# Performance work log

Hardware: AMD Instinct MI355X
Metric: run time of the kernel (lower is better)

Reference implementation:

```python
import jax, jax.numpy as jnp
import numpy as np

B, N, C, H, M = 32, 256, 1024, 16, 77
DH = C // H
W = int(N ** 0.5)
MLP_H = 4 * C

def _rel_index(w):
    ch = np.arange(w)
    coords = np.stack(np.meshgrid(ch, ch, indexing='ij'))  # [2, w, w]
    cf = coords.reshape(2, -1)
    rc = (cf[:, :, None] - cf[:, None, :]).transpose(1, 2, 0).astype(np.int64)
    rc[..., 0] += w - 1
    rc[..., 1] += w - 1
    rc[..., 0] *= 2 * w - 1
    return jnp.asarray(rc.sum(-1))  # [N, N]

REL_IDX = _rel_index(W)

def setup_inputs():
    key = jax.random.key(0)
    ks = jax.random.split(key, 12)
    p = lambda k, sh: jax.random.normal(k, sh, jnp.float32) * 0.02
    return dict(
        x=jax.random.normal(ks[0], (B, N, C), jnp.float32),
        noise_level=jax.random.normal(ks[1], (B, C), jnp.float32),
        y=jax.random.normal(ks[2], (B, M, C), jnp.float32),
        W_qkv=p(ks[3], (C, 3 * C)), b_qkv=jnp.zeros((3 * C,), jnp.float32),
        W_proj=p(ks[4], (C, C)), b_proj=jnp.zeros((C,), jnp.float32),
        rel_table=p(ks[5], ((2 * W - 1) ** 2 + 3, H)),
        W_ada=p(ks[6], (C, 6 * C)), b_ada=jnp.zeros((6 * C,), jnp.float32),
        W_fc1=p(ks[7], (C, MLP_H)), b_fc1=jnp.zeros((MLP_H,), jnp.float32),
        W_fc2=p(ks[8], (MLP_H, C)), b_fc2=jnp.zeros((C,), jnp.float32),
        W_q=p(ks[9], (C, C)), W_kv=p(ks[10], (C, 2 * C)),
    )

def _ln(x):
    # LayerNorm without affine, eps=1e-6, biased variance (matches torch)
    mu = x.mean(-1, keepdims=True)
    var = x.var(-1, keepdims=True)
    return (x - mu) * jax.lax.rsqrt(var + 1e-6)

def _modulate(x, shift, scale):
    return x * (1 + scale[:, None, :]) + shift[:, None, :]

def reference(x, noise_level, y, W_qkv, b_qkv, W_proj, b_proj, rel_table,
              W_ada, b_ada, W_fc1, b_fc1, W_fc2, b_fc2, W_q, W_kv):
    ada = jax.nn.silu(noise_level) @ W_ada + b_ada  # [B, 6C]
    sh_msa, sc_msa, g_msa, sh_mlp, sc_mlp, g_mlp = jnp.split(ada, 6, axis=1)

    # --- self-attention with relative position bias (heads split as (h d)) ---
    h = _modulate(_ln(x), sh_msa, sc_msa)
    qkv = (h @ W_qkv + b_qkv).reshape(B, N, 3, H, DH)
    q, k, v = qkv[:, :, 0], qkv[:, :, 1], qkv[:, :, 2]  # [B, N, H, DH]
    bias = rel_table[REL_IDX].transpose(2, 0, 1)  # [H, N, N]
    scores = jnp.einsum('bnhd,bmhd->bhnm', q, k) * (DH ** -0.5) + bias[None]
    attn = jax.nn.softmax(scores, axis=-1)
    o = jnp.einsum('bhnm,bmhd->bnhd', attn, v).reshape(B, N, C)
    x = x + g_msa[:, None, :] * (o @ W_proj + b_proj)

    # --- cross attention; einops '(d h)' split: head index is the FAST axis ---
    q2 = (x @ W_q).reshape(B, N, DH, H)
    kv = y @ W_kv
    k2 = kv[..., :C].reshape(B, M, DH, H)
    v2 = kv[..., C:].reshape(B, M, DH, H)
    s2 = jnp.einsum('bndh,bmdh->bhnm', q2, k2) * (DH ** -0.5)
    a2 = jax.nn.softmax(s2, axis=-1)
    o2 = jnp.einsum('bhnm,bmdh->bndh', a2, v2).reshape(B, N, C)
    x = x + o2

    # --- adaLN-modulated MLP with tanh-approx GELU ---
    h = _modulate(_ln(x), sh_mlp, sc_mlp)
    h = jax.nn.gelu(h @ W_fc1 + b_fc1, approximate=True) @ W_fc2 + b_fc2
    return x + g_mlp[:, None, :] * h
```

## Files before the change

kernel.cpp:

```cpp
#include <hip/hip_runtime.h>
#include <hip/hip_bf16.h>
#include <stdint.h>

typedef __hip_bfloat16 bf16;
using bf16x8 = __attribute__((ext_vector_type(8))) short;
using f32x4  = __attribute__((ext_vector_type(4))) float;


__device__ __forceinline__ void gload_lds16(const void* g, void* l) {
  using gchar = __attribute__((address_space(1))) char;
  using lchar = __attribute__((address_space(3))) char;
  gchar* gp = reinterpret_cast<gchar*>(reinterpret_cast<uintptr_t>(g));
  lchar* lp = reinterpret_cast<lchar*>(static_cast<uint32_t>(reinterpret_cast<uintptr_t>(l)));
  __builtin_amdgcn_global_load_lds(gp, lp, 16, 0, 0);
}

__device__ __forceinline__ unsigned short f2bf_bits(float x) {
  uint32_t u = __float_as_uint(x);
  uint32_t r = (u + 0x7fffu + ((u >> 16) & 1u)) >> 16;
  return (unsigned short)r;
}

template <int PERM>
__global__ __launch_bounds__(256) void transpose_bf16(
    const float* __restrict__ W, bf16* __restrict__ Wt, int K, int N) {
  __shared__ float t[32][33];
  const int n0 = blockIdx.x * 32, k0 = blockIdx.y * 32;
  const int tx = threadIdx.x & 31, ty = threadIdx.x >> 5;
  #pragma unroll
  for (int i = ty; i < 32; i += 8) t[i][tx] = W[(size_t)(k0 + i) * N + n0 + tx];
  __syncthreads();
  #pragma unroll
  for (int i = ty; i < 32; i += 8) {
    int n = n0 + i;
    int np;
    if constexpr (PERM == 0) np = n;
    else if constexpr (PERM == 1) np = (n & 15) * 64 + (n >> 4);
    else { int base = n & 1024, m = n & 1023; np = base + (m & 15) * 64 + (m >> 4); }
    Wt[(size_t)np * K + k0 + tx] = __float2bfloat16(t[tx][i]);
  }
}

__global__ __launch_bounds__(256) void conv_y(
    const float* __restrict__ y, bf16* __restrict__ yb) {
  int i = blockIdx.x * 256 + threadIdx.x;
  float v = (i < 2464 * 1024) ? y[i] : 0.f;
  yb[i] = __float2bfloat16(v);
}

__global__ __launch_bounds__(256) void silu_pad(
    const float* __restrict__ noise, bf16* __restrict__ Apad) {
  int i = blockIdx.x * 256 + threadIdx.x;
  float v = 0.f;
  if (i < 32 * 1024) {
    float x = noise[i];
    v = x / (1.f + __expf(-x));
  }
  Apad[i] = __float2bfloat16(v);
}

__global__ __launch_bounds__(256) void ln_mod(
    const float* __restrict__ x, const float* __restrict__ ada,
    int shOff, int scOff, bf16* __restrict__ out) {
  const int row = blockIdx.x, b = row >> 8, tid = threadIdx.x;
  const float* xr = x + (size_t)row * 1024;
  float v[4], s = 0.f, ss = 0.f;
  #pragma unroll
  for (int i = 0; i < 4; ++i) {
    v[i] = xr[tid + i * 256];
    s += v[i]; ss += v[i] * v[i];
  }
  #pragma unroll
  for (int o = 32; o; o >>= 1) { s += __shfl_xor(s, o); ss += __shfl_xor(ss, o); }
  __shared__ float red[8];
  const int w = tid >> 6;
  if ((tid & 63) == 0) { red[w] = s; red[w + 4] = ss; }
  __syncthreads();
  s = red[0] + red[1] + red[2] + red[3];
  ss = red[4] + red[5] + red[6] + red[7];
  float mu = s * (1.f / 1024.f);
  float var = ss * (1.f / 1024.f) - mu * mu;
  float rstd = rsqrtf(var + 1e-6f);
  const float* adab = ada + (size_t)b * 6144;
  #pragma unroll
  for (int i = 0; i < 4; ++i) {
    int c = tid + i * 256;
    float o = (v[i] - mu) * rstd * (1.f + adab[scOff + c]) + adab[shOff + c];
    out[(size_t)row * 1024 + c] = __float2bfloat16(o);
  }
}

enum { EPI_STORE = 0, EPI_GELU = 1, EPI_PROJ = 2, EPI_OUT = 3, EPI_ADAF = 4 };

template <int EPI>
__global__ __launch_bounds__(256, 2) void gemm_bf16(
    const bf16* __restrict__ A, const bf16* __restrict__ Bt,
    int N, int K, int gx, int grpG, int xcdP,
    const float* __restrict__ bias, const float* __restrict__ ada, int adaOff,
    const float* __restrict__ resid, float* __restrict__ outF,
    bf16* __restrict__ outB) {
  __shared__ bf16 As[128 * 64];
  __shared__ bf16 Bs[128 * 64];
  const int tid = threadIdx.x;
  const int w = tid >> 6, lane = tid & 63;
  const int wr = w >> 1, wc = w & 1;
  const int lr = lane >> 4, lc = lane & 15;

  const int flat = blockIdx.x;
  const int xcd = flat & 7, j = flat >> 3;
  const int cpg = gx / grpG;
  const int grp = xcd / xcdP, par = xcd % xcdP;
  const int bx = grp * cpg + j % cpg;
  const int by = (j / cpg) * xcdP + par;
  const int mBase = by * 128, nBase = bx * 128;

  f32x4 acc[4][4];
  #pragma unroll
  for (int mi = 0; mi < 4; ++mi)
    #pragma unroll
    for (int ni = 0; ni < 4; ++ni)
      #pragma unroll
      for (int j2 = 0; j2 < 4; ++j2) acc[mi][ni][j2] = 0.f;

  const int nK = K >> 6;
  for (int ks = 0; ks < nK; ++ks) {
    const int k0 = ks << 6;
    #pragma unroll
    for (int i = 0; i < 4; ++i) {
      int t16 = w * 256 + i * 64 + lane;
      int row = t16 >> 3;
      int cL = ((t16 & 7) ^ (row & 7)) << 3;
      gload_lds16(A + (size_t)(mBase + row) * K + k0 + cL, (char*)As + t16 * 16);
      gload_lds16(Bt + (size_t)(nBase + row) * K + k0 + cL, (char*)Bs + t16 * 16);
    }
    __syncthreads();
    #pragma unroll
    for (int kk = 0; kk < 2; ++kk) {
      bf16x8 af[4], bfr[4];
      #pragma unroll
      for (int mi = 0; mi < 4; ++mi) {
        int row = wr * 64 + mi * 16 + lc;
        int byte = row * 128 + ((kk * 64 + lr * 16) ^ ((row & 7) << 4));
        af[mi] = *reinterpret_cast<const bf16x8*>((const char*)As + byte);
      }
      #pragma unroll
      for (int ni = 0; ni < 4; ++ni) {
        int row = wc * 64 + ni * 16 + lc;
        int byte = row * 128 + ((kk * 64 + lr * 16) ^ ((row & 7) << 4));
        bfr[ni] = *reinterpret_cast<const bf16x8*>((const char*)Bs + byte);
      }
      #pragma unroll
      for (int mi = 0; mi < 4; ++mi)
        #pragma unroll
        for (int ni = 0; ni < 4; ++ni)
          acc[mi][ni] = __builtin_amdgcn_mfma_f32_16x16x32_bf16(
              af[mi], bfr[ni], acc[mi][ni], 0, 0, 0);
    }
    __syncthreads();
  }

  const int rB = mBase + wr * 64, cB = nBase + wc * 64;
  #pragma unroll
  for (int mi = 0; mi < 4; ++mi) {
    #pragma unroll
    for (int ni = 0; ni < 4; ++ni) {
      #pragma unroll
      for (int j2 = 0; j2 < 4; ++j2) {
        int r = rB + mi * 16 + lr * 4 + j2;
        int c = cB + ni * 16 + lc;
        float v = acc[mi][ni][j2];
        if (bias) v += bias[c];
        if constexpr (EPI == EPI_STORE) {
          outB[(size_t)r * N + c] = __float2bfloat16(v);
        } else if constexpr (EPI == EPI_GELU) {
          float e = __expf(1.5957691216057308f * v + 0.07135481627260086f * v * v * v);
          float t = 1.f - 2.f / (e + 1.f);
          outB[(size_t)r * N + c] = __float2bfloat16(0.5f * v * (1.f + t));
        } else if constexpr (EPI == EPI_PROJ) {
          int b = r >> 8;
          float g = ada[(size_t)b * 6144 + adaOff + c];
          float o = resid[(size_t)r * 1024 + c] + g * v;
          outF[(size_t)r * 1024 + c] = o;
          outB[(size_t)r * 1024 + c] = __float2bfloat16(o);
        } else if constexpr (EPI == EPI_OUT) {
          int b = r >> 8;
          float g = ada[(size_t)b * 6144 + adaOff + c];
          outF[(size_t)r * 1024 + c] = resid[(size_t)r * 1024 + c] + g * v;
        } else {
          if (r < 32) outF[(size_t)r * N + c] = v;
        }
      }
    }
  }
}

template <int EPI>
__global__ __launch_bounds__(512, 1) void gemm256_bf16(
    const bf16* __restrict__ A, const bf16* __restrict__ Bt,
    int N, int K, int gx, int grpG, int xcdP,
    const float* __restrict__ bias, bf16* __restrict__ outB) {
  __shared__ bf16 As[2 * 256 * 64];
  __shared__ bf16 Bs[2 * 256 * 64];
  const int tid = threadIdx.x;
  const int w = tid >> 6, lane = tid & 63;
  const int wr = w >> 2, wcn = w & 3;
  const int lr = lane >> 4, lc = lane & 15;

  const int flat = blockIdx.x;
  const int xcd = flat & 7, jj = flat >> 3;
  const int cpg = gx / grpG;
  const int grp = xcd / xcdP, par = xcd % xcdP;
  const int bx = grp * cpg + jj % cpg;
  const int by = (jj / cpg) * xcdP + par;
  const int mBase = by * 256, nBase = bx * 256;

  f32x4 acc[8][4];
  #pragma unroll
  for (int mi = 0; mi < 8; ++mi)
    #pragma unroll
    for (int ni = 0; ni < 4; ++ni)
      acc[mi][ni] = f32x4{0.f, 0.f, 0.f, 0.f};

  const int nT = K >> 6;

  auto STAGE = [&](int t, int bufI) {
    const int k0 = t << 6;
    char* Ad = (char*)As + bufI * 32768;
    char* Bd = (char*)Bs + bufI * 32768;
    #pragma unroll
    for (int i = 0; i < 4; ++i) {
      int ck = i * 512 + tid;
      int row = ck >> 3;
      int sc = ((ck & 7) ^ (row & 7)) << 3;
      gload_lds16(A + (size_t)(mBase + row) * K + k0 + sc, Ad + ck * 16);
      gload_lds16(Bt + (size_t)(nBase + row) * K + k0 + sc, Bd + ck * 16);
    }
  };

  STAGE(0, 0);
  STAGE(1, 1);
  asm volatile("s_waitcnt vmcnt(8)" ::: "memory");
  __builtin_amdgcn_sched_barrier(0);
  __builtin_amdgcn_s_barrier();
  __builtin_amdgcn_sched_barrier(0);

  for (int t = 0; t < nT; ++t) {
    const int cur = t & 1;
    const char* Ab = (const char*)As + cur * 32768;
    const char* Bb = (const char*)Bs + cur * 32768;
    bf16x8 af[2][8], bfr[2][4];
    #pragma unroll
    for (int kk = 0; kk < 2; ++kk) {
      #pragma unroll
      for (int mi = 0; mi < 8; ++mi) {
        int row = wr * 128 + mi * 16 + lc;
        int byte = row * 128 + ((kk * 64 + lr * 16) ^ ((row & 7) << 4));
        af[kk][mi] = *reinterpret_cast<const bf16x8*>(Ab + byte);
      }
      #pragma unroll
      for (int ni = 0; ni < 4; ++ni) {
        int row = wcn * 64 + ni * 16 + lc;
        int byte = row * 128 + ((kk * 64 + lr * 16) ^ ((row & 7) << 4));
        bfr[kk][ni] = *reinterpret_cast<const bf16x8*>(Bb + byte);
      }
    }
    asm volatile("s_waitcnt lgkmcnt(0)" ::: "memory");
    __builtin_amdgcn_sched_barrier(0);
    __builtin_amdgcn_s_barrier();
    __builtin_amdgcn_sched_barrier(0);

    if (t + 2 < nT) STAGE(t + 2, cur);

    __builtin_amdgcn_s_setprio(1);
    #pragma unroll
    for (int kk = 0; kk < 2; ++kk)
      #pragma unroll
      for (int mi = 0; mi < 8; ++mi)
        #pragma unroll
        for (int ni = 0; ni < 4; ++ni)
          acc[mi][ni] = __builtin_amdgcn_mfma_f32_16x16x32_bf16(
              af[kk][mi], bfr[kk][ni], acc[mi][ni], 0, 0, 0);
    __builtin_amdgcn_s_setprio(0);

    if (t < nT - 1) {
      if (t + 2 < nT) {
        asm volatile("s_waitcnt vmcnt(8)" ::: "memory");
      } else {
        asm volatile("s_waitcnt vmcnt(0)" ::: "memory");
      }
      __builtin_amdgcn_sched_barrier(0);
      __builtin_amdgcn_s_barrier();
      __builtin_amdgcn_sched_barrier(0);
    }
  }

  const int rB = mBase + wr * 128, cB = nBase + wcn * 64;
  #pragma unroll
  for (int mi = 0; mi < 8; ++mi) {
    #pragma unroll
    for (int ni = 0; ni < 4; ++ni) {
      #pragma unroll
      for (int j2 = 0; j2 < 4; ++j2) {
        int r = rB + mi * 16 + lr * 4 + j2;
        int c = cB + ni * 16 + lc;
        float v = acc[mi][ni][j2] + bias[c];
        if constexpr (EPI == EPI_STORE) {
          outB[(size_t)r * N + c] = __float2bfloat16(v);
        } else {
          float e = __expf(1.5957691216057308f * v + 0.07135481627260086f * v * v * v);
          float t2 = 1.f - 2.f / (e + 1.f);
          outB[(size_t)r * N + c] = __float2bfloat16(0.5f * v * (1.f + t2));
        }
      }
    }
  }
}

__global__ __launch_bounds__(512, 1) void attn1_mfma(
    const bf16* __restrict__ qkv, const float* __restrict__ rel,
    bf16* __restrict__ o) {
  __shared__ bf16 Ks[256 * 64];
  __shared__ bf16 Vt[64 * 256];
  __shared__ ushort Pl[8][32 * 40];
  __shared__ float bias_s[964];

  const int tid = threadIdx.x;
  const int w = tid >> 6, lane = tid & 63;
  const int p4 = lane >> 4, c = lane & 15;
  const int bh = blockIdx.x, b = bh >> 4, h = bh & 15;
  const bf16* basep = qkv + (size_t)b * 256 * 3072 + h * 64;

  #pragma unroll
  for (int it = 0; it < 4; ++it) {
    int t16 = it * 512 + tid;
    int row = t16 >> 3;
    int sc = ((t16 & 7) ^ (row & 7)) << 3;
    gload_lds16(basep + (size_t)row * 3072 + 1024 + sc, (char*)Ks + t16 * 16);
  }
  #pragma unroll
  for (int it = 0; it < 4; ++it) {
    int i = it * 512 + tid;
    int key = i >> 3, d0 = (i & 7) * 8;
    int4 u = *reinterpret_cast<const int4*>(basep + (size_t)key * 3072 + 2048 + d0);
    const ushort* us = reinterpret_cast<const ushort*>(&u);
    #pragma unroll
    for (int j = 0; j < 8; ++j) {
      int dh = d0 + j;
      int byte = dh * 512 + ((key * 2) ^ ((dh & 7) << 4));
      *reinterpret_cast<ushort*>((char*)Vt + byte) = us[j];
    }
  }
  for (int i = tid; i < 964; i += 512) bias_s[i] = rel[i * 16 + h];

  bf16x8 qf[2][2];
  #pragma unroll
  for (int mi = 0; mi < 2; ++mi)
    #pragma unroll
    for (int s = 0; s < 2; ++s) {
      int q = w * 32 + mi * 16 + c;
      int dh = s * 32 + p4 * 8;
      int4 u = *reinterpret_cast<const int4*>(basep + (size_t)q * 3072 + dh);
      uint32_t a[4] = {(uint32_t)u.x, (uint32_t)u.y, (uint32_t)u.z, (uint32_t)u.w};
      bf16x8 r;
      #pragma unroll
      for (int t = 0; t < 4; ++t) {
        float lo = __uint_as_float(a[t] << 16) * 0.125f;
        float hi = __uint_as_float(a[t] & 0xffff0000u) * 0.125f;
        r[2 * t]     = (short)(__float_as_uint(lo) >> 16);
        r[2 * t + 1] = (short)(__float_as_uint(hi) >> 16);
      }
      qf[mi][s] = r;
    }
  __syncthreads();

  float m_run[2][4], l_run[2][4];
  f32x4 oacc[2][4];
  #pragma unroll
  for (int mi = 0; mi < 2; ++mi)
    #pragma unroll
    for (int j = 0; j < 4; ++j) {
      m_run[mi][j] = -1e30f; l_run[mi][j] = 0.f;
      oacc[mi][j] = f32x4{0.f, 0.f, 0.f, 0.f};
    }

  ushort* Pw = &Pl[w][0];
  const int colterm = p4 * 4 - c + 15;

  for (int kt = 0; kt < 8; ++kt) {
    f32x4 sacc[2][2];
    #pragma unroll
    for (int mi = 0; mi < 2; ++mi)
      #pragma unroll
      for (int nf = 0; nf < 2; ++nf) {
        int bi = ((w * 2 + mi) - (kt * 2 + nf) + 15) * 31 + colterm;
        #pragma unroll
        for (int j = 0; j < 4; ++j) sacc[mi][nf][j] = bias_s[bi + j];
      }
    #pragma unroll
    for (int nf = 0; nf < 2; ++nf) {
      int key = kt * 32 + nf * 16 + c;
      #pragma unroll
      for (int s = 0; s < 2; ++s) {
        int byte = key * 128 + (((s * 4 + p4) ^ (key & 7)) << 4);
        bf16x8 kb = *reinterpret_cast<const bf16x8*>((const char*)Ks + byte);
        #pragma unroll
        for (int mi = 0; mi < 2; ++mi)
          sacc[mi][nf] = __builtin_amdgcn_mfma_f32_16x16x32_bf16(
              qf[mi][s], kb, sacc[mi][nf], 0, 0, 0);
      }
    }
    float sf[2][4];
    #pragma unroll
    for (int mi = 0; mi < 2; ++mi)
      #pragma unroll
      for (int j = 0; j < 4; ++j) {
        float cm = fmaxf(sacc[mi][0][j], sacc[mi][1][j]);
        cm = fmaxf(cm, __shfl_xor(cm, 1));
        cm = fmaxf(cm, __shfl_xor(cm, 2));
        cm = fmaxf(cm, __shfl_xor(cm, 4));
        cm = fmaxf(cm, __shfl_xor(cm, 8));
        float nm = fmaxf(m_run[mi][j], cm);
        sf[mi][j] = __expf(m_run[mi][j] - nm);
        m_run[mi][j] = nm;
        l_run[mi][j] *= sf[mi][j];
      }
    #pragma unroll
    for (int mi = 0; mi < 2; ++mi)
      #pragma unroll
      for (int nf = 0; nf < 4; ++nf)
        #pragma unroll
        for (int j = 0; j < 4; ++j) oacc[mi][nf][j] *= sf[mi][j];
    #pragma unroll
    for (int mi = 0; mi < 2; ++mi) {
      #pragma unroll
      for (int nf = 0; nf < 2; ++nf)
        #pragma unroll
        for (int j = 0; j < 4; ++j)
          sacc[mi][nf][j] = __expf(sacc[mi][nf][j] - m_run[mi][j]);
      #pragma unroll
      for (int j = 0; j < 4; ++j) {
        float lp = sacc[mi][0][j] + sacc[mi][1][j];
        lp += __shfl_xor(lp, 1);
        lp += __shfl_xor(lp, 2);
        lp += __shfl_xor(lp, 4);
        lp += __shfl_xor(lp, 8);
        l_run[mi][j] += lp;
      }
      #pragma unroll
      for (int nf = 0; nf < 2; ++nf)
        #pragma unroll
        for (int j = 0; j < 4; ++j)
          Pw[(mi * 16 + p4 * 4 + j) * 40 + nf * 16 + c] =
              f2bf_bits(sacc[mi][nf][j]);
    }
    bf16x8 pa[2], vb[4];
    #pragma unroll
    for (int mi = 0; mi < 2; ++mi)
      pa[mi] = *reinterpret_cast<const bf16x8*>(
          (const char*)Pw + (mi * 16 + c) * 80 + p4 * 16);
    #pragma unroll
    for (int nf = 0; nf < 4; ++nf) {
      int dh = nf * 16 + c;
      int byte = dh * 512 + (((kt * 4 + p4) ^ (dh & 7)) << 4);
      vb[nf] = *reinterpret_cast<const bf16x8*>((const char*)Vt + byte);
    }
    #pragma unroll
    for (int mi = 0; mi < 2; ++mi)
      #pragma unroll
      for (int nf = 0; nf < 4; ++nf)
        oacc[mi][nf] = __builtin_amdgcn_mfma_f32_16x16x32_bf16(
            pa[mi], vb[nf], oacc[mi][nf], 0, 0, 0);
  }

  #pragma unroll
  for (int mi = 0; mi < 2; ++mi) {
    float inv[4];
    #pragma unroll
    for (int j = 0; j < 4; ++j) inv[j] = 1.f / l_run[mi][j];
    #pragma unroll
    for (int nf = 0; nf < 4; ++nf)
      #pragma unroll
      for (int j = 0; j < 4; ++j) {
        int q = w * 32 + mi * 16 + p4 * 4 + j;
        int dh = nf * 16 + c;
        o[((size_t)b * 256 + q) * 1024 + h * 64 + dh] =
            __float2bfloat16(oacc[mi][nf][j] * inv[j]);
      }
  }
}

__global__ __launch_bounds__(512, 1) void attn2_mfma(
    const bf16* __restrict__ q2, const bf16* __restrict__ kv,
    bf16* __restrict__ o2) {
  __shared__ bf16 Ks[80 * 64];
  __shared__ bf16 Vt[64 * 128];
  __shared__ ushort Pl[8][32 * 104];

  const int tid = threadIdx.x;
  const int w = tid >> 6, lane = tid & 63;
  const int p4 = lane >> 4, c = lane & 15;
  const int bh = blockIdx.x, b = bh >> 4, h = bh & 15;
  const size_t kvrow0 = (size_t)b * 77;

  {
    int t16 = tid;
    int key = t16 >> 3;
    int sc = ((t16 & 7) ^ (key & 7)) << 3;
    gload_lds16(kv + (kvrow0 + key) * 2048 + h * 64 + sc, (char*)Ks + t16 * 16);
    if (tid < 128) {
      int u16 = 512 + tid; key = u16 >> 3;
      sc = ((u16 & 7) ^ (key & 7)) << 3;
      gload_lds16(kv + (kvrow0 + key) * 2048 + h * 64 + sc, (char*)Ks + u16 * 16);
    }
  }
  for (int i = tid; i < 80 * 8; i += 512) {
    int key = i >> 3, d0 = (i & 7) * 8;
    int4 u = *reinterpret_cast<const int4*>(
        kv + (kvrow0 + key) * 2048 + 1024 + h * 64 + d0);
    const ushort* us = reinterpret_cast<const ushort*>(&u);
    #pragma unroll
    for (int j = 0; j < 8; ++j) {
      int dh = d0 + j;
      int byte = dh * 256 + ((key * 2) ^ ((dh & 7) << 4));
      *reinterpret_cast<ushort*>((char*)Vt + byte) = us[j];
    }
  }
  {
    int row = lane >> 1, colb = 160 + (lane & 1) * 16;
    *reinterpret_cast<int4*>((char*)&Pl[w][0] + row * 208 + colb) =
        int4{0, 0, 0, 0};
  }
  bf16x8 qf[2][2];
  #pragma unroll
  for (int mi = 0; mi < 2; ++mi)
    #pragma unroll
    for (int s = 0; s < 2; ++s) {
      int q = w * 32 + mi * 16 + c;
      int dh = s * 32 + p4 * 8;
      int4 u = *reinterpret_cast<const int4*>(
          q2 + ((size_t)b * 256 + q) * 1024 + h * 64 + dh);
      uint32_t a[4] = {(uint32_t)u.x, (uint32_t)u.y, (uint32_t)u.z, (uint32_t)u.w};
      bf16x8 r;
      #pragma unroll
      for (int t = 0; t < 4; ++t) {
        float lo = __uint_as_float(a[t] << 16) * 0.125f;
        float hi = __uint_as_float(a[t] & 0xffff0000u) * 0.125f;
        r[2 * t]     = (short)(__float_as_uint(lo) >> 16);
        r[2 * t + 1] = (short)(__float_as_uint(hi) >> 16);
      }
      qf[mi][s] = r;
    }
  __syncthreads();

  f32x4 sacc[2][5];
  #pragma unroll
  for (int mi = 0; mi < 2; ++mi)
    #pragma unroll
    for (int nf = 0; nf < 5; ++nf)
      sacc[mi][nf] = f32x4{0.f, 0.f, 0.f, 0.f};
  #pragma unroll
  for (int nf = 0; nf < 5; ++nf) {
    int key = nf * 16 + c;
    #pragma unroll
    for (int s = 0; s < 2; ++s) {
      int byte = key * 128 + (((s * 4 + p4) ^ (key & 7)) << 4);
      bf16x8 kb = *reinterpret_cast<const bf16x8*>((const char*)Ks + byte);
      #pragma unroll
      for (int mi = 0; mi < 2; ++mi)
        sacc[mi][nf] = __builtin_amdgcn_mfma_f32_16x16x32_bf16(
            qf[mi][s], kb, sacc[mi][nf], 0, 0, 0);
    }
  }
  if (c >= 13) {
    #pragma unroll
    for (int mi = 0; mi < 2; ++mi)
      #pragma unroll
      for (int j = 0; j < 4; ++j) sacc[mi][4][j] = -1e30f;
  }
  float lrow[2][4];
  #pragma unroll
  for (int mi = 0; mi < 2; ++mi)
    #pragma unroll
    for (int j = 0; j < 4; ++j) {
      float cm = sacc[mi][0][j];
      #pragma unroll
      for (int nf = 1; nf < 5; ++nf) cm = fmaxf(cm, sacc[mi][nf][j]);
      cm = fmaxf(cm, __shfl_xor(cm, 1));
      cm = fmaxf(cm, __shfl_xor(cm, 2));
      cm = fmaxf(cm, __shfl_xor(cm, 4));
      cm = fmaxf(cm, __shfl_xor(cm, 8));
      float lp = 0.f;
      #pragma unroll
      for (int nf = 0; nf < 5; ++nf) {
        sacc[mi][nf][j] = __expf(sacc[mi][nf][j] - cm);
        lp += sacc[mi][nf][j];
      }
      lp += __shfl_xor(lp, 1);
      lp += __shfl_xor(lp, 2);
      lp += __shfl_xor(lp, 4);
      lp += __shfl_xor(lp, 8);
      lrow[mi][j] = lp;
    }
  ushort* Pw = &Pl[w][0];
  #pragma unroll
  for (int mi = 0; mi < 2; ++mi)
    #pragma unroll
    for (int nf = 0; nf < 5; ++nf)
      #pragma unroll
      for (int j = 0; j < 4; ++j)
        Pw[(mi * 16 + p4 * 4 + j) * 104 + nf * 16 + c] =
            f2bf_bits(sacc[mi][nf][j]);
  f32x4 oacc[2][4];
  #pragma unroll
  for (int mi = 0; mi < 2; ++mi)
    #pragma unroll
    for (int nf = 0; nf < 4; ++nf) oacc[mi][nf] = f32x4{0.f, 0.f, 0.f, 0.f};
  #pragma unroll
  for (int kk = 0; kk < 3; ++kk) {
    bf16x8 pa[2], vb[4];
    #pragma unroll
    for (int mi = 0; mi < 2; ++mi)
      pa[mi] = *reinterpret_cast<const bf16x8*>(
          (const char*)Pw + (mi * 16 + c) * 208 + kk * 64 + p4 * 16);
    #pragma unroll
    for (int nf = 0; nf < 4; ++nf) {
      int dh = nf * 16 + c;
      int byte = dh * 256 + (((kk * 4 + p4) ^ (dh & 7)) << 4);
      vb[nf] = *reinterpret_cast<const bf16x8*>((const char*)Vt + byte);
    }
    #pragma unroll
    for (int mi = 0; mi < 2; ++mi)
      #pragma unroll
      for (int nf = 0; nf < 4; ++nf)
        oacc[mi][nf] = __builtin_amdgcn_mfma_f32_16x16x32_bf16(
            pa[mi], vb[nf], oacc[mi][nf], 0, 0, 0);
  }
  #pragma unroll
  for (int mi = 0; mi < 2; ++mi) {
    float inv[4];
    #pragma unroll
    for (int j = 0; j < 4; ++j) inv[j] = 1.f / lrow[mi][j];
    #pragma unroll
    for (int nf = 0; nf < 4; ++nf)
      #pragma unroll
      for (int j = 0; j < 4; ++j) {
        int q = w * 32 + mi * 16 + p4 * 4 + j;
        int dh = nf * 16 + c;
        o2[((size_t)b * 256 + q) * 1024 + h * 64 + dh] =
            __float2bfloat16(oacc[mi][nf][j] * inv[j]);
      }
  }
}

__global__ __launch_bounds__(256) void permute_add(
    const bf16* __restrict__ o2, float* __restrict__ xcur) {
  __shared__ float s_lds[1088];
  const int tid = threadIdx.x;
  const int row0 = blockIdx.x * 4;
  for (int r = 0; r < 4; ++r) {
    const int row = row0 + r;
    #pragma unroll
    for (int i = 0; i < 4; ++i) {
      int cc = i * 256 + tid;
      float v = __bfloat162float(o2[(size_t)row * 1024 + cc]);
      s_lds[cc + (cc >> 4)] = v;
    }
    __syncthreads();
    float4 add;
    #pragma unroll
    for (int t = 0; t < 4; ++t) {
      int ct = tid * 4 + t;
      int src = (ct & 15) * 64 + (ct >> 4);
      (&add.x)[t] = s_lds[src + (src >> 4)];
    }
    float4* xp = reinterpret_cast<float4*>(xcur + (size_t)row * 1024 + tid * 4);
    float4 cur = *xp;
    cur.x += add.x; cur.y += add.y; cur.z += add.z; cur.w += add.w;
    *xp = cur;
    __syncthreads();
  }
}


extern "C" void kernel_launch(void* const* d_in, const int* in_sizes, int n_in,
                              void* d_out, int out_size, void* d_ws, size_t ws_size,
                              hipStream_t stream) {
  (void)in_sizes; (void)n_in; (void)out_size; (void)ws_size;
  const float* x      = (const float*)d_in[0];
  const float* noise  = (const float*)d_in[1];
  const float* y      = (const float*)d_in[2];
  const float* W_qkv  = (const float*)d_in[3];
  const float* b_qkv  = (const float*)d_in[4];
  const float* W_proj = (const float*)d_in[5];
  const float* b_proj = (const float*)d_in[6];
  const float* rel    = (const float*)d_in[7];
  const float* W_ada  = (const float*)d_in[8];
  const float* b_ada  = (const float*)d_in[9];
  const float* W_fc1  = (const float*)d_in[10];
  const float* b_fc1  = (const float*)d_in[11];
  const float* W_fc2  = (const float*)d_in[12];
  const float* b_fc2  = (const float*)d_in[13];
  const float* W_q    = (const float*)d_in[14];
  const float* W_kv   = (const float*)d_in[15];

  char* ws = (char*)d_ws;
  size_t off = 0;
  auto alloc = [&](size_t bytes) {
    char* p = ws + off;
    off = (off + bytes + 255) & ~(size_t)255;
    return p;
  };
  float* ada   = (float*)alloc(32u * 6144 * 4);
  float* xcur  = (float*)alloc(8192u * 1024 * 4);
  bf16* WqkvT  = (bf16*)alloc(3072u * 1024 * 2);
  bf16* WprojT = (bf16*)alloc(1024u * 1024 * 2);
  bf16* WqT    = (bf16*)alloc(1024u * 1024 * 2);
  bf16* WkvT   = (bf16*)alloc(2048u * 1024 * 2);
  bf16* Wfc1T  = (bf16*)alloc(4096u * 1024 * 2);
  bf16* Wfc2T  = (bf16*)alloc(1024u * 4096 * 2);
  bf16* WadaT  = (bf16*)alloc(6144u * 1024 * 2);
  bf16* Apad   = (bf16*)alloc(128u * 1024 * 2);
  bf16* hbuf   = (bf16*)alloc(8192u * 1024 * 2);
  bf16* big    = (bf16*)alloc(8192u * 4096 * 2);
  bf16* obuf   = (bf16*)alloc(8192u * 1024 * 2);
  bf16* kvbuf  = (bf16*)alloc(2560u * 2048 * 2);
  bf16* ybuf   = (bf16*)alloc(2560u * 1024 * 2);
  float* outF  = (float*)d_out;

  transpose_bf16<0><<<dim3(96, 32), 256, 0, stream>>>(W_qkv, WqkvT, 1024, 3072);
  transpose_bf16<0><<<dim3(32, 32), 256, 0, stream>>>(W_proj, WprojT, 1024, 1024);
  transpose_bf16<1><<<dim3(32, 32), 256, 0, stream>>>(W_q, WqT, 1024, 1024);
  transpose_bf16<2><<<dim3(64, 32), 256, 0, stream>>>(W_kv, WkvT, 1024, 2048);
  transpose_bf16<0><<<dim3(128, 32), 256, 0, stream>>>(W_fc1, Wfc1T, 1024, 4096);
  transpose_bf16<0><<<dim3(32, 128), 256, 0, stream>>>(W_fc2, Wfc2T, 4096, 1024);
  transpose_bf16<0><<<dim3(192, 32), 256, 0, stream>>>(W_ada, WadaT, 1024, 6144);
  conv_y<<<2560 * 1024 / 256, 256, 0, stream>>>(y, ybuf);

  silu_pad<<<512, 256, 0, stream>>>(noise, Apad);
  gemm_bf16<EPI_ADAF><<<48, 256, 0, stream>>>(
      Apad, WadaT, 6144, 1024, 48, 8, 1, b_ada, nullptr, 0, nullptr, ada, nullptr);

  ln_mod<<<8192, 256, 0, stream>>>(x, ada, 0, 1024, hbuf);
  gemm256_bf16<EPI_STORE><<<384, 512, 0, stream>>>(
      hbuf, WqkvT, 3072, 1024, 12, 4, 2, b_qkv, big);
  attn1_mfma<<<512, 512, 0, stream>>>(big, rel, obuf);
  gemm_bf16<EPI_PROJ><<<512, 256, 0, stream>>>(
      obuf, WprojT, 1024, 1024, 8, 1, 8, b_proj, ada, 2048, x, xcur, hbuf);

  gemm_bf16<EPI_STORE><<<512, 256, 0, stream>>>(
      hbuf, WqT, 1024, 1024, 8, 1, 8, nullptr, nullptr, 0, nullptr, nullptr, obuf);
  gemm_bf16<EPI_STORE><<<320, 256, 0, stream>>>(
      ybuf, WkvT, 2048, 1024, 16, 8, 1, nullptr, nullptr, 0, nullptr, nullptr, kvbuf);
  attn2_mfma<<<512, 512, 0, stream>>>(obuf, kvbuf, big);
  permute_add<<<2048, 256, 0, stream>>>(big, xcur);

  ln_mod<<<8192, 256, 0, stream>>>(xcur, ada, 3072, 4096, hbuf);
  gemm256_bf16<EPI_GELU><<<512, 512, 0, stream>>>(
      hbuf, Wfc1T, 4096, 1024, 16, 4, 2, b_fc1, big);
  gemm_bf16<EPI_OUT><<<512, 256, 0, stream>>>(
      big, Wfc2T, 1024, 4096, 8, 1, 8, b_fc2, ada, 5120, xcur, outF, nullptr);
}
```

Before: 518.1 us.

## Replace 256-tile GEMM with 8-phase interleaved pipeline and reuse it for proj/fc2

Rewrites the 256x256 bf16 GEMM as a templated kernel that splits each K-tile's A and B loads into four half-tile stages. Those stages are interleaved with four MFMA quarter-phases separated by barriers, so global-to-LDS traffic overlaps compute at finer granularity. The kernel also gets a 256x128 variant (NI=2) with the PROJ/OUT/STORE epilogues, replacing the older 256-thread gemm for the proj, q and fc2 GEMMs. The intent is better latency hiding and larger tiles with more reuse, at the cost of many more barriers and fewer blocks for the N=1024 GEMMs.

```diff
diff --git a/kernel.cpp b/kernel.cpp
--- a/kernel.cpp
+++ b/kernel.cpp
@@ -194,122 +194,193 @@
   }
 }
 
-template <int EPI>
-__global__ __launch_bounds__(512, 1) void gemm256_bf16(
+template <int EPI, int NI>
+__global__ __launch_bounds__(512, 1) void gemm8p(
     const bf16* __restrict__ A, const bf16* __restrict__ Bt,
     int N, int K, int gx, int grpG, int xcdP,
-    const float* __restrict__ bias, bf16* __restrict__ outB) {
-  __shared__ bf16 As[2 * 256 * 64];
-  __shared__ bf16 Bs[2 * 256 * 64];
+    const float* __restrict__ bias, const float* __restrict__ ada, int adaOff,
+    const float* __restrict__ resid, float* __restrict__ outF,
+    bf16* __restrict__ outB) {
+  constexpr int BHALF = NI * 32;
+  constexpr int NB_LOADS = NI / 2;
+  __shared__ bf16 AS[2 * 2 * 128 * 64];
+  __shared__ bf16 BS[2 * 2 * BHALF * 64];
+
   const int tid = threadIdx.x;
   const int w = tid >> 6, lane = tid & 63;
-  const int wr = w >> 2, wcn = w & 3;
+  const int wr = w >> 2, wc = w & 3;
   const int lr = lane >> 4, lc = lane & 15;
 
   const int flat = blockIdx.x;
   const int xcd = flat & 7, jj = flat >> 3;
   const int cpg = gx / grpG;
-  const int grp = xcd / xcdP, par = xcd % xcdP;
+  const int grp = xcd / xcdP, par_ = xcd % xcdP;
   const int bx = grp * cpg + jj % cpg;
-  const int by = (jj / cpg) * xcdP + par;
-  const int mBase = by * 256, nBase = bx * 256;
-
-  f32x4 acc[8][4];
+  const int by = (jj / cpg) * xcdP + par_;
+  const int mBase = by * 256, nBase = bx * (NI * 64);
+
+  const int nT = K >> 6;
+
+  f32x4 acc[8][NI];
   #pragma unroll
   for (int mi = 0; mi < 8; ++mi)
     #pragma unroll
-    for (int ni = 0; ni < 4; ++ni)
-      acc[mi][ni] = f32x4{0.f, 0.f, 0.f, 0.f};
-
-  const int nT = K >> 6;
-
-  auto STAGE = [&](int t, int bufI) {
-    const int k0 = t << 6;
-    char* Ad = (char*)As + bufI * 32768;
-    char* Bd = (char*)Bs + bufI * 32768;
-    #pragma unroll
-    for (int i = 0; i < 4; ++i) {
-      int ck = i * 512 + tid;
-      int row = ck >> 3;
-      int sc = ((ck & 7) ^ (row & 7)) << 3;
-      gload_lds16(A + (size_t)(mBase + row) * K + k0 + sc, Ad + ck * 16);
-      gload_lds16(Bt + (size_t)(nBase + row) * K + k0 + sc, Bd + ck * 16);
+    for (int ni = 0; ni < NI; ++ni) acc[mi][ni] = f32x4{0.f, 0.f, 0.f, 0.f};
+
+  auto STAGE = [&](int h) {
+    if (h >= 4 * nT) return;
+    const int th = h >> 2, j = h & 3, par = th & 1;
+    const int k0 = th << 6;
+    if (j < 2) {
+      char* dst = (char*)AS + par * 32768 + j * 16384;
+      #pragma unroll
+      for (int i = 0; i < 2; ++i) {
+        int ck = i * 512 + tid;
+        int row = ck >> 3, c = ck & 7;
+        int col = k0 + ((c ^ (row & 7)) << 3);
+        gload_lds16(A + (size_t)(mBase + j * 128 + row) * K + col, dst + ck * 16);
+      }
+    } else {
+      const int rh = j - 2;
+      char* dst = (char*)BS + par * (BHALF * 256) + rh * (BHALF * 128);
+      #pragma unroll
+      for (int i = 0; i < NB_LOADS; ++i) {
+        int ck = i * 512 + tid;
+        int row = ck >> 3, c = ck & 7;
+        int col = k0 + ((c ^ (row & 7)) << 3);
+        gload_lds16(Bt + (size_t)(nBase + rh * BHALF + row) * K + col, dst + ck * 16);
+      }
     }
   };
 
-  STAGE(0, 0);
-  STAGE(1, 1);
-  asm volatile("s_waitcnt vmcnt(8)" ::: "memory");
-  __builtin_amdgcn_sched_barrier(0);
-  __builtin_amdgcn_s_barrier();
-  __builtin_amdgcn_sched_barrier(0);
+  STAGE(0); STAGE(1); STAGE(2); STAGE(3); STAGE(4); STAGE(5);
 
   for (int t = 0; t < nT; ++t) {
-    const int cur = t & 1;
-    const char* Ab = (const char*)As + cur * 32768;
-    const char* Bb = (const char*)Bs + cur * 32768;
-    bf16x8 af[2][8], bfr[2][4];
-    #pragma unroll
-    for (int kk = 0; kk < 2; ++kk) {
-      #pragma unroll
-      for (int mi = 0; mi < 8; ++mi) {
-        int row = wr * 128 + mi * 16 + lc;
-        int byte = row * 128 + ((kk * 64 + lr * 16) ^ ((row & 7) << 4));
-        af[kk][mi] = *reinterpret_cast<const bf16x8*>(Ab + byte);
-      }
-      #pragma unroll
-      for (int ni = 0; ni < 4; ++ni) {
-        int row = wcn * 64 + ni * 16 + lc;
-        int byte = row * 128 + ((kk * 64 + lr * 16) ^ ((row & 7) << 4));
-        bfr[kk][ni] = *reinterpret_cast<const bf16x8*>(Bb + byte);
-      }
-    }
+    if (t == nT - 1) { asm volatile("s_waitcnt vmcnt(0)" ::: "memory"); }
+    else            { asm volatile("s_waitcnt vmcnt(4)" ::: "memory"); }
+    __builtin_amdgcn_sched_barrier(0);
+    __builtin_amdgcn_s_barrier();
+    __builtin_amdgcn_sched_barrier(0);
+
+    const char* Ab = (const char*)AS + (t & 1) * 32768 + wr * 16384;
+    const char* Bb = (const char*)BS + (t & 1) * (BHALF * 256) + (wc >> 1) * (BHALF * 128);
+
+    bf16x8 af[2][8], bfr[2][NI];
+
+    #pragma unroll
+    for (int mi = 0; mi < 8; ++mi) {
+      int r = mi * 16 + lc;
+      af[0][mi] = *reinterpret_cast<const bf16x8*>(
+          Ab + r * 128 + ((lr * 16) ^ ((r & 7) << 4)));
+    }
+    #pragma unroll
+    for (int ni = 0; ni < NI; ++ni) {
+      int r = (wc * (NI * 16) + ni * 16 + lc) & (BHALF - 1);
+      bfr[0][ni] = *reinterpret_cast<const bf16x8*>(
+          Bb + r * 128 + ((lr * 16) ^ ((r & 7) << 4)));
+    }
+    STAGE(4 * t + 6);
+    __builtin_amdgcn_sched_barrier(0);
+    __builtin_amdgcn_s_barrier();
     asm volatile("s_waitcnt lgkmcnt(0)" ::: "memory");
     __builtin_amdgcn_sched_barrier(0);
+    __builtin_amdgcn_s_setprio(1);
+    #pragma unroll
+    for (int mi = 0; mi < 8; ++mi)
+      #pragma unroll
+      for (int ni = 0; ni < NI / 2; ++ni)
+        acc[mi][ni] = __builtin_amdgcn_mfma_f32_16x16x32_bf16(
+            af[0][mi], bfr[0][ni], acc[mi][ni], 0, 0, 0);
+    __builtin_amdgcn_s_setprio(0);
+    __builtin_amdgcn_sched_barrier(0);
     __builtin_amdgcn_s_barrier();
-    __builtin_amdgcn_sched_barrier(0);
-
-    if (t + 2 < nT) STAGE(t + 2, cur);
-
+
+    #pragma unroll
+    for (int mi = 0; mi < 8; ++mi) {
+      int r = mi * 16 + lc;
+      af[1][mi] = *reinterpret_cast<const bf16x8*>(
+          Ab + r * 128 + ((64 + lr * 16) ^ ((r & 7) << 4)));
+    }
+    #pragma unroll
+    for (int ni = 0; ni < NI; ++ni) {
+      int r = (wc * (NI * 16) + ni * 16 + lc) & (BHALF - 1);
+      bfr[1][ni] = *reinterpret_cast<const bf16x8*>(
+          Bb + r * 128 + ((64 + lr * 16) ^ ((r & 7) << 4)));
+    }
+    STAGE(4 * t + 7);
+    __builtin_amdgcn_sched_barrier(0);
+    __builtin_amdgcn_s_barrier();
+    asm volatile("s_waitcnt lgkmcnt(0)" ::: "memory");
+    __builtin_amdgcn_sched_barrier(0);
     __builtin_amdgcn_s_setprio(1);
     #pragma unroll
-    for (int kk = 0; kk < 2; ++kk)
-      #pragma unroll
-      for (int mi = 0; mi < 8; ++mi)
-        #pragma unroll
-        for (int ni = 0; ni < 4; ++ni)
-          acc[mi][ni] = __builtin_amdgcn_mfma_f32_16x16x32_bf16(
-              af[kk][mi], bfr[kk][ni], acc[mi][ni], 0, 0, 0);
+    for (int mi = 0; mi < 8; ++mi)
+      #pragma unroll
+      for (int ni = NI / 2; ni < NI; ++ni)
+        acc[mi][ni] = __builtin_amdgcn_mfma_f32_16x16x32_bf16(
+            af[0][mi], bfr[0][ni], acc[mi][ni], 0, 0, 0);
     __builtin_amdgcn_s_setprio(0);
-
-    if (t < nT - 1) {
-      if (t + 2 < nT) {
-        asm volatile("s_waitcnt vmcnt(8)" ::: "memory");
-      } else {
-        asm volatile("s_waitcnt vmcnt(0)" ::: "memory");
-      }
-      __builtin_amdgcn_sched_barrier(0);
-      __builtin_amdgcn_s_barrier();
-      __builtin_amdgcn_sched_barrier(0);
-    }
-  }
-
-  const int rB = mBase + wr * 128, cB = nBase + wcn * 64;
+    __builtin_amdgcn_sched_barrier(0);
+    __builtin_amdgcn_s_barrier();
+
+    STAGE(4 * t + 8);
+    __builtin_amdgcn_sched_barrier(0);
+    __builtin_amdgcn_s_barrier();
+    __builtin_amdgcn_sched_barrier(0);
+    __builtin_amdgcn_s_setprio(1);
+    #pragma unroll
+    for (int mi = 0; mi < 8; ++mi)
+      #pragma unroll
+      for (int ni = 0; ni < NI / 2; ++ni)
+        acc[mi][ni] = __builtin_amdgcn_mfma_f32_16x16x32_bf16(
+            af[1][mi], bfr[1][ni], acc[mi][ni], 0, 0, 0);
+    __builtin_amdgcn_s_setprio(0);
+    __builtin_amdgcn_sched_barrier(0);
+    __builtin_amdgcn_s_barrier();
+
+    STAGE(4 * t + 9);
+    __builtin_amdgcn_sched_barrier(0);
+    __builtin_amdgcn_s_barrier();
+    __builtin_amdgcn_sched_barrier(0);
+    __builtin_amdgcn_s_setprio(1);
+    #pragma unroll
+    for (int mi = 0; mi < 8; ++mi)
+      #pragma unroll
+      for (int ni = NI / 2; ni < NI; ++ni)
+        acc[mi][ni] = __builtin_amdgcn_mfma_f32_16x16x32_bf16(
+            af[1][mi], bfr[1][ni], acc[mi][ni], 0, 0, 0);
+    __builtin_amdgcn_s_setprio(0);
+    __builtin_amdgcn_sched_barrier(0);
+    __builtin_amdgcn_s_barrier();
+  }
+
+  const int rB = mBase + wr * 128, cB = nBase + wc * (NI * 16);
   #pragma unroll
   for (int mi = 0; mi < 8; ++mi) {
     #pragma unroll
-    for (int ni = 0; ni < 4; ++ni) {
+    for (int ni = 0; ni < NI; ++ni) {
       #pragma unroll
       for (int j2 = 0; j2 < 4; ++j2) {
         int r = rB + mi * 16 + lr * 4 + j2;
         int c = cB + ni * 16 + lc;
-        float v = acc[mi][ni][j2] + bias[c];
+        float v = acc[mi][ni][j2];
+        if (bias) v += bias[c];
         if constexpr (EPI == EPI_STORE) {
           outB[(size_t)r * N + c] = __float2bfloat16(v);
-        } else {
+        } else if constexpr (EPI == EPI_GELU) {
           float e = __expf(1.5957691216057308f * v + 0.07135481627260086f * v * v * v);
           float t2 = 1.f - 2.f / (e + 1.f);
           outB[(size_t)r * N + c] = __float2bfloat16(0.5f * v * (1.f + t2));
+        } else if constexpr (EPI == EPI_PROJ) {
+          int b = r >> 8;
+          float g = ada[(size_t)b * 6144 + adaOff + c];
+          float o = resid[(size_t)r * 1024 + c] + g * v;
+          outF[(size_t)r * 1024 + c] = o;
+          outB[(size_t)r * 1024 + c] = __float2bfloat16(o);
+        } else if constexpr (EPI == EPI_OUT) {
+          int b = r >> 8;
+          float g = ada[(size_t)b * 6144 + adaOff + c];
+          outF[(size_t)r * 1024 + c] = resid[(size_t)r * 1024 + c] + g * v;
         }
       }
     }
@@ -741,13 +812,13 @@
       Apad, WadaT, 6144, 1024, 48, 8, 1, b_ada, nullptr, 0, nullptr, ada, nullptr);
 
   ln_mod<<<8192, 256, 0, stream>>>(x, ada, 0, 1024, hbuf);
-  gemm256_bf16<EPI_STORE><<<384, 512, 0, stream>>>(
-      hbuf, WqkvT, 3072, 1024, 12, 4, 2, b_qkv, big);
+  gemm8p<EPI_STORE, 4><<<384, 512, 0, stream>>>(
+      hbuf, WqkvT, 3072, 1024, 12, 4, 2, b_qkv, nullptr, 0, nullptr, nullptr, big);
   attn1_mfma<<<512, 512, 0, stream>>>(big, rel, obuf);
-  gemm_bf16<EPI_PROJ><<<512, 256, 0, stream>>>(
+  gemm8p<EPI_PROJ, 2><<<256, 512, 0, stream>>>(
       obuf, WprojT, 1024, 1024, 8, 1, 8, b_proj, ada, 2048, x, xcur, hbuf);
 
-  gemm_bf16<EPI_STORE><<<512, 256, 0, stream>>>(
+  gemm8p<EPI_STORE, 2><<<256, 512, 0, stream>>>(
       hbuf, WqT, 1024, 1024, 8, 1, 8, nullptr, nullptr, 0, nullptr, nullptr, obuf);
   gemm_bf16<EPI_STORE><<<320, 256, 0, stream>>>(
       ybuf, WkvT, 2048, 1024, 16, 8, 1, nullptr, nullptr, 0, nullptr, nullptr, kvbuf);
@@ -755,8 +826,8 @@
   permute_add<<<2048, 256, 0, stream>>>(big, xcur);
 
   ln_mod<<<8192, 256, 0, stream>>>(xcur, ada, 3072, 4096, hbuf);
-  gemm256_bf16<EPI_GELU><<<512, 512, 0, stream>>>(
-      hbuf, Wfc1T, 4096, 1024, 16, 4, 2, b_fc1, big);
-  gemm_bf16<EPI_OUT><<<512, 256, 0, stream>>>(
+  gemm8p<EPI_GELU, 4><<<512, 512, 0, stream>>>(
+      hbuf, Wfc1T, 4096, 1024, 16, 4, 2, b_fc1, nullptr, 0, nullptr, nullptr, big);
+  gemm8p<EPI_OUT, 2><<<256, 512, 0, stream>>>(
       big, Wfc2T, 1024, 4096, 8, 1, 8, b_fc2, ada, 5120, xcur, outF, nullptr);
 }
```

Result: slower. 580.0 us (+12.0%).

## Restructure 256x256 GEMM main loop into four interleaved quadrant stages

Applied to the files above, without the earlier changes.

The 256x256 bf16 GEMM used for QKV and FC1 now splits each K-tile's A and B into two halves each. The loop runs four MFMA quadrant phases, with LDS fragment reads and global-to-LDS prefetches of the next halves placed between them. This replaces the bulk load-then-compute pattern with finer-grained overlap of memory traffic and matrix math, in the style of 8-wave ping-pong schedules. The cost is many more workgroup barriers per iteration and more complex vmcnt accounting, which could stall if the waits are mistuned.

```diff
diff --git a/kernel.cpp b/kernel.cpp
--- a/kernel.cpp
+++ b/kernel.cpp
@@ -195,106 +195,168 @@
 }
 
 template <int EPI>
-__global__ __launch_bounds__(512, 1) void gemm256_bf16(
+__global__ __launch_bounds__(512, 1) void gemm8q(
     const bf16* __restrict__ A, const bf16* __restrict__ Bt,
     int N, int K, int gx, int grpG, int xcdP,
     const float* __restrict__ bias, bf16* __restrict__ outB) {
-  __shared__ bf16 As[2 * 256 * 64];
-  __shared__ bf16 Bs[2 * 256 * 64];
+  __shared__ bf16 AS[2][2][128 * 64];
+  __shared__ bf16 BS[2][2][128 * 64];
   const int tid = threadIdx.x;
   const int w = tid >> 6, lane = tid & 63;
-  const int wr = w >> 2, wcn = w & 3;
+  const int wr = w >> 2, wc = w & 3;
   const int lr = lane >> 4, lc = lane & 15;
 
   const int flat = blockIdx.x;
   const int xcd = flat & 7, jj = flat >> 3;
   const int cpg = gx / grpG;
-  const int grp = xcd / xcdP, par = xcd % xcdP;
+  const int grp = xcd / xcdP, par_ = xcd % xcdP;
   const int bx = grp * cpg + jj % cpg;
-  const int by = (jj / cpg) * xcdP + par;
+  const int by = (jj / cpg) * xcdP + par_;
   const int mBase = by * 256, nBase = bx * 256;
+  const int nT = K >> 6;
 
   f32x4 acc[8][4];
   #pragma unroll
   for (int mi = 0; mi < 8; ++mi)
     #pragma unroll
-    for (int ni = 0; ni < 4; ++ni)
-      acc[mi][ni] = f32x4{0.f, 0.f, 0.f, 0.f};
-
-  const int nT = K >> 6;
-
-  auto STAGE = [&](int t, int bufI) {
-    const int k0 = t << 6;
-    char* Ad = (char*)As + bufI * 32768;
-    char* Bd = (char*)Bs + bufI * 32768;
-    #pragma unroll
-    for (int i = 0; i < 4; ++i) {
+    for (int ni = 0; ni < 4; ++ni) acc[mi][ni] = f32x4{0.f, 0.f, 0.f, 0.f};
+
+  auto STAGE_A = [&](int th, int h) {
+    if (th >= nT) return;
+    const int k0 = th << 6;
+    char* dst = (char*)&AS[th & 1][h][0];
+    #pragma unroll
+    for (int i = 0; i < 2; ++i) {
       int ck = i * 512 + tid;
-      int row = ck >> 3;
-      int sc = ((ck & 7) ^ (row & 7)) << 3;
-      gload_lds16(A + (size_t)(mBase + row) * K + k0 + sc, Ad + ck * 16);
-      gload_lds16(Bt + (size_t)(nBase + row) * K + k0 + sc, Bd + ck * 16);
+      int rr = ck >> 3, c = ck & 7;
+      int grow = mBase + (rr & 63) + ((rr >> 6) << 7) + h * 64;
+      gload_lds16(A + (size_t)grow * K + k0 + ((c ^ (rr & 7)) << 3), dst + ck * 16);
     }
   };
-
-  STAGE(0, 0);
-  STAGE(1, 1);
-  asm volatile("s_waitcnt vmcnt(8)" ::: "memory");
-  __builtin_amdgcn_sched_barrier(0);
-  __builtin_amdgcn_s_barrier();
-  __builtin_amdgcn_sched_barrier(0);
+  auto STAGE_B = [&](int th, int h) {
+    if (th >= nT) return;
+    const int k0 = th << 6;
+    char* dst = (char*)&BS[th & 1][h][0];
+    #pragma unroll
+    for (int i = 0; i < 2; ++i) {
+      int ck = i * 512 + tid;
+      int rr = ck >> 3, c = ck & 7;
+      int grow = nBase + ((rr >> 5) << 6) + h * 32 + (rr & 31);
+      gload_lds16(Bt + (size_t)grow * K + k0 + ((c ^ (rr & 7)) << 3), dst + ck * 16);
+    }
+  };
+
+  STAGE_A(0, 0); STAGE_A(0, 1); STAGE_B(0, 0); STAGE_B(0, 1);
+  STAGE_A(1, 0); STAGE_A(1, 1);
 
   for (int t = 0; t < nT; ++t) {
-    const int cur = t & 1;
-    const char* Ab = (const char*)As + cur * 32768;
-    const char* Bb = (const char*)Bs + cur * 32768;
-    bf16x8 af[2][8], bfr[2][4];
+    if (t == nT - 1) { asm volatile("s_waitcnt vmcnt(0)" ::: "memory"); }
+    else             { asm volatile("s_waitcnt vmcnt(4)" ::: "memory"); }
+    __builtin_amdgcn_s_barrier();
+
+    const int p = t & 1;
+    const char* A0 = (const char*)&AS[p][0][0];
+    const char* A1 = (const char*)&AS[p][1][0];
+    const char* B0 = (const char*)&BS[p][0][0];
+    const char* B1 = (const char*)&BS[p][1][0];
+
+    bf16x8 af0[2][4], af1[2][4], bf01[2][2], bf23[2][2];
+
     #pragma unroll
     for (int kk = 0; kk < 2; ++kk) {
       #pragma unroll
-      for (int mi = 0; mi < 8; ++mi) {
-        int row = wr * 128 + mi * 16 + lc;
-        int byte = row * 128 + ((kk * 64 + lr * 16) ^ ((row & 7) << 4));
-        af[kk][mi] = *reinterpret_cast<const bf16x8*>(Ab + byte);
-      }
-      #pragma unroll
-      for (int ni = 0; ni < 4; ++ni) {
-        int row = wcn * 64 + ni * 16 + lc;
-        int byte = row * 128 + ((kk * 64 + lr * 16) ^ ((row & 7) << 4));
-        bfr[kk][ni] = *reinterpret_cast<const bf16x8*>(Bb + byte);
-      }
-    }
+      for (int mi = 0; mi < 4; ++mi) {
+        int rr = wr * 64 + mi * 16 + lc;
+        af0[kk][mi] = *reinterpret_cast<const bf16x8*>(
+            A0 + rr * 128 + ((kk * 64 + lr * 16) ^ ((rr & 7) << 4)));
+      }
+      #pragma unroll
+      for (int ni = 0; ni < 2; ++ni) {
+        int rr = wc * 32 + ni * 16 + lc;
+        bf01[kk][ni] = *reinterpret_cast<const bf16x8*>(
+            B0 + rr * 128 + ((kk * 64 + lr * 16) ^ ((rr & 7) << 4)));
+      }
+    }
+    STAGE_B(t + 1, 0);
+    __builtin_amdgcn_s_barrier();
     asm volatile("s_waitcnt lgkmcnt(0)" ::: "memory");
     __builtin_amdgcn_sched_barrier(0);
+    __builtin_amdgcn_s_setprio(1);
+    #pragma unroll
+    for (int kk = 0; kk < 2; ++kk)
+      #pragma unroll
+      for (int mi = 0; mi < 4; ++mi)
+        #pragma unroll
+        for (int ni = 0; ni < 2; ++ni)
+          acc[mi][ni] = __builtin_amdgcn_mfma_f32_16x16x32_bf16(
+              af0[kk][mi], bf01[kk][ni], acc[mi][ni], 0, 0, 0);
+    __builtin_amdgcn_s_setprio(0);
     __builtin_amdgcn_s_barrier();
+
+    #pragma unroll
+    for (int kk = 0; kk < 2; ++kk)
+      #pragma unroll
+      for (int ni = 0; ni < 2; ++ni) {
+        int rr = wc * 32 + ni * 16 + lc;
+        bf23[kk][ni] = *reinterpret_cast<const bf16x8*>(
+            B1 + rr * 128 + ((kk * 64 + lr * 16) ^ ((rr & 7) << 4)));
+      }
+    STAGE_B(t + 1, 1);
+    __builtin_amdgcn_s_barrier();
+    asm volatile("s_waitcnt lgkmcnt(0)" ::: "memory");
     __builtin_amdgcn_sched_barrier(0);
-
-    if (t + 2 < nT) STAGE(t + 2, cur);
-
     __builtin_amdgcn_s_setprio(1);
     #pragma unroll
     for (int kk = 0; kk < 2; ++kk)
       #pragma unroll
-      for (int mi = 0; mi < 8; ++mi)
-        #pragma unroll
-        for (int ni = 0; ni < 4; ++ni)
-          acc[mi][ni] = __builtin_amdgcn_mfma_f32_16x16x32_bf16(
-              af[kk][mi], bfr[kk][ni], acc[mi][ni], 0, 0, 0);
+      for (int mi = 0; mi < 4; ++mi)
+        #pragma unroll
+        for (int ni = 0; ni < 2; ++ni)
+          acc[mi][ni + 2] = __builtin_amdgcn_mfma_f32_16x16x32_bf16(
+              af0[kk][mi], bf23[kk][ni], acc[mi][ni + 2], 0, 0, 0);
     __builtin_amdgcn_s_setprio(0);
-
-    if (t < nT - 1) {
-      if (t + 2 < nT) {
-        asm volatile("s_waitcnt vmcnt(8)" ::: "memory");
-      } else {
-        asm volatile("s_waitcnt vmcnt(0)" ::: "memory");
-      }
-      __builtin_amdgcn_sched_barrier(0);
-      __builtin_amdgcn_s_barrier();
-      __builtin_amdgcn_sched_barrier(0);
-    }
-  }
-
-  const int rB = mBase + wr * 128, cB = nBase + wcn * 64;
+    __builtin_amdgcn_s_barrier();
+
+    #pragma unroll
+    for (int kk = 0; kk < 2; ++kk)
+      #pragma unroll
+      for (int mi = 0; mi < 4; ++mi) {
+        int rr = wr * 64 + mi * 16 + lc;
+        af1[kk][mi] = *reinterpret_cast<const bf16x8*>(
+            A1 + rr * 128 + ((kk * 64 + lr * 16) ^ ((rr & 7) << 4)));
+      }
+    STAGE_A(t + 2, 0);
+    __builtin_amdgcn_s_barrier();
+    asm volatile("s_waitcnt lgkmcnt(0)" ::: "memory");
+    __builtin_amdgcn_sched_barrier(0);
+    __builtin_amdgcn_s_setprio(1);
+    #pragma unroll
+    for (int kk = 0; kk < 2; ++kk)
+      #pragma unroll
+      for (int mi = 0; mi < 4; ++mi)
+        #pragma unroll
+        for (int ni = 0; ni < 2; ++ni)
+          acc[mi + 4][ni] = __builtin_amdgcn_mfma_f32_16x16x32_bf16(
+              af1[kk][mi], bf01[kk][ni], acc[mi + 4][ni], 0, 0, 0);
+    __builtin_amdgcn_s_setprio(0);
+    __builtin_amdgcn_s_barrier();
+
+    STAGE_A(t + 2, 1);
+    __builtin_amdgcn_s_barrier();
+    __builtin_amdgcn_s_setprio(1);
+    #pragma unroll
+    for (int kk = 0; kk < 2; ++kk)
+      #pragma unroll
+      for (int mi = 0; mi < 4; ++mi)
+        #pragma unroll
+        for (int ni = 0; ni < 2; ++ni)
+          acc[mi + 4][ni + 2] = __builtin_amdgcn_mfma_f32_16x16x32_bf16(
+              af1[kk][mi], bf23[kk][ni], acc[mi + 4][ni + 2], 0, 0, 0);
+    __builtin_amdgcn_s_setprio(0);
+    __builtin_amdgcn_s_barrier();
+  }
+
+  const int rB = mBase + wr * 128, cB = nBase + wc * 64;
   #pragma unroll
   for (int mi = 0; mi < 8; ++mi) {
     #pragma unroll
@@ -741,7 +803,7 @@
       Apad, WadaT, 6144, 1024, 48, 8, 1, b_ada, nullptr, 0, nullptr, ada, nullptr);
 
   ln_mod<<<8192, 256, 0, stream>>>(x, ada, 0, 1024, hbuf);
-  gemm256_bf16<EPI_STORE><<<384, 512, 0, stream>>>(
+  gemm8q<EPI_STORE><<<384, 512, 0, stream>>>(
       hbuf, WqkvT, 3072, 1024, 12, 4, 2, b_qkv, big);
   attn1_mfma<<<512, 512, 0, stream>>>(big, rel, obuf);
   gemm_bf16<EPI_PROJ><<<512, 256, 0, stream>>>(
@@ -755,7 +817,7 @@
   permute_add<<<2048, 256, 0, stream>>>(big, xcur);
 
   ln_mod<<<8192, 256, 0, stream>>>(xcur, ada, 3072, 4096, hbuf);
-  gemm256_bf16<EPI_GELU><<<512, 512, 0, stream>>>(
+  gemm8q<EPI_GELU><<<512, 512, 0, stream>>>(
       hbuf, Wfc1T, 4096, 1024, 16, 4, 2, b_fc1, big);
   gemm_bf16<EPI_OUT><<<512, 256, 0, stream>>>(
       big, Wfc2T, 1024, 4096, 8, 1, 8, b_fc2, ada, 5120, xcur, outF, nullptr);
```

After: 513.6 us. No clear change (-0.9%).
